# Kernel tuning notes

Measured on AMD Instinct MI355X. Metric: run time of the kernel, lower is better.

## Reference

```python
import jax, jax.numpy as jnp
import numpy as np

HEADS = 16
ROPE_BASE = 10000.0


def _rope(x):
    # x: [b, h, n, d]. lucidrains partial rotary: RotaryEmbedding(head_dim//2)
    # rotates only the first rot_dim = d//2 channels, interleaved-pair style.
    d = x.shape[-1]
    rot = d // 2
    inv_freq = 1.0 / (ROPE_BASE ** (jnp.arange(0, rot, 2, dtype=jnp.float32) / rot))  # [rot//2]
    pos = jnp.arange(x.shape[2], dtype=jnp.float32)
    freqs = pos[:, None] * inv_freq[None, :]                  # [n, rot//2]
    cos, sin = jnp.cos(freqs), jnp.sin(freqs)
    xr, xp = x[..., :rot], x[..., rot:]
    x1, x2 = xr[..., 0::2], xr[..., 1::2]                     # interleaved pairs
    o1 = x1 * cos - x2 * sin
    o2 = x2 * cos + x1 * sin
    xr_out = jnp.stack([o1, o2], axis=-1).reshape(xr.shape)   # re-interleave
    return jnp.concatenate([xr_out, xp], axis=-1)


def setup_inputs() -> dict:
    key = jax.random.key(0)
    k0, k1 = jax.random.split(key)
    B, N, D = 2, 2048, 2048
    x = jax.random.normal(k0, (B, N, D), dtype=jnp.float32)
    W_qkv = jax.random.normal(k1, (3 * D, D), dtype=jnp.float32) * (D ** -0.5)
    b_qkv = jnp.zeros((3 * D,), dtype=jnp.float32)
    return {"x": x, "W_qkv": W_qkv, "b_qkv": b_qkv}


def reference(x, W_qkv, b_qkv):
    B, N, D = x.shape
    H = HEADS
    hd = D // H
    qkv = x @ W_qkv.T + b_qkv                                  # [b, n, 3d]
    q, k, v = jnp.split(qkv, 3, axis=-1)
    to_heads = lambda t: t.reshape(B, N, H, hd).transpose(0, 2, 1, 3)  # b h n d
    q, k, v = to_heads(q), to_heads(k), to_heads(v)
    q, k = _rope(q), _rope(k)
    scale = 1.0 / np.sqrt(hd)
    scores = jnp.einsum('bhnd,bhmd->bhnm', q, k) * scale
    causal = jnp.tril(jnp.ones((N, N), dtype=bool))
    scores = jnp.where(causal, scores, -jnp.inf)
    attn = jax.nn.softmax(scores, axis=-1)
    y = jnp.einsum('bhnm,bhmd->bhnd', attn, v)
    return y.transpose(0, 2, 1, 3).reshape(B, N, D)
```

## Files before the change

kernel.cpp:

```cpp
#include <hip/hip_runtime.h>
#include <hip/hip_bf16.h>
#include <math.h>

typedef unsigned short u16;
typedef unsigned int u32;
typedef __attribute__((ext_vector_type(8))) short bf16x8;
typedef __attribute__((ext_vector_type(4))) float f32x4;

#define B_ 2
#define N_ 2048
#define D_ 2048
#define H_ 16
#define HD 128
#define GK 2048

__device__ __forceinline__ u16 f2bf(float f) {
  u32 u = __float_as_uint(f);
  u = (u + 0x7fffu + ((u >> 16) & 1u)) >> 16;
  return (u16)u;
}

__device__ __forceinline__ u32 cvtpk(float lo, float hi) {
  u32 r;
  asm("v_cvt_pk_bf16_f32 %0, %1, %2" : "=v"(r) : "v"(lo), "v"(hi));
  return r;
}

__device__ __forceinline__ void gload_lds16(const void* g, void* l) {
  __builtin_amdgcn_global_load_lds(
      (const __attribute__((address_space(1))) u32*)g,
      (__attribute__((address_space(3))) u32*)l, 16, 0, 0);
}

__global__ __launch_bounds__(256) void prep_kernel(
    const float* __restrict__ x, const float* __restrict__ Wq,
    u16* __restrict__ Xb, u16* __restrict__ Wb, float* __restrict__ tbl) {
  const int i0 = blockIdx.x * blockDim.x + threadIdx.x;
  const int st = gridDim.x * blockDim.x;
  const int n4x = (B_ * N_ * D_) / 4;
  const int n4w = (3 * D_ * D_) / 4;
  for (int i = i0; i < n4x + n4w; i += st) {
    float4 v;
    ushort4 o;
    if (i < n4x) {
      v = ((const float4*)x)[i];
      o.x = f2bf(v.x); o.y = f2bf(v.y); o.z = f2bf(v.z); o.w = f2bf(v.w);
      ((ushort4*)Xb)[i] = o;
    } else {
      v = ((const float4*)Wq)[i - n4x];
      o.x = f2bf(v.x); o.y = f2bf(v.y); o.z = f2bf(v.z); o.w = f2bf(v.w);
      ((ushort4*)Wb)[i - n4x] = o;
    }
  }
  for (int i = i0; i < N_ * 32; i += st) {
    int pos = i >> 5, p = i & 31;
    double inv = pow(10000.0, -(double)p / 32.0);
    double a = (double)pos * inv;
    tbl[2 * i]     = (float)cos(a);
    tbl[2 * i + 1] = (float)sin(a);
  }
}

__global__ __launch_bounds__(256, 2) void qkv_gemm_kernel(
    const u16* __restrict__ X, const u16* __restrict__ W,
    const float* __restrict__ bias, const float* __restrict__ tbl,
    u16* __restrict__ Qo, u16* __restrict__ Ko, u16* __restrict__ Vo) {
  __shared__ char smem[81920];
  const int tid = threadIdx.x;
  const int lane = tid & 63;
  const int w = tid >> 6;
  const int l15 = lane & 15, l4 = lane >> 4;

  const int bid = blockIdx.x;
  const int i_ = bid >> 3;
  const int m0 = (i_ >> 2) * 128;
  const int n0 = ((bid & 7) * 4 + (i_ & 3)) * 192;

  const int aof0 = (l4 * 16) ^ ((l15 & 7) << 4);
  const int aof1 = (64 + l4 * 16) ^ ((l15 & 7) << 4);

  int soRow[6], soCol[6];
#pragma unroll
  for (int c = 0; c < 6; ++c) {
    int o = c * 4096 + tid * 16;
    int lo = o ^ (((o >> 7) & 7) << 4);
    soRow[c] = lo >> 7;
    soCol[c] = (lo & 127) >> 1;
  }

  f32x4 acc[8][3];
#pragma unroll
  for (int fm = 0; fm < 8; ++fm)
#pragma unroll
    for (int fn = 0; fn < 3; ++fn)
#pragma unroll
      for (int q = 0; q < 4; ++q) acc[fm][fn][q] = 0.f;

  auto stageA = [&](char* Ab, int k0) {
#pragma unroll
    for (int c = 0; c < 4; ++c)
      gload_lds16(X + (size_t)(m0 + soRow[c]) * GK + k0 + soCol[c],
                  Ab + c * 4096 + tid * 16);
  };
  auto stageB = [&](char* Bb, int k0) {
#pragma unroll
    for (int c = 0; c < 6; ++c)
      gload_lds16(W + (size_t)(n0 + soRow[c]) * GK + k0 + soCol[c],
                  Bb + c * 4096 + tid * 16);
  };

  const int NK = GK / 64;

  stageA(smem, 0);
  stageB(smem + 32768, 0);
  asm volatile("s_waitcnt vmcnt(0)" ::: "memory");
  __builtin_amdgcn_s_barrier();

  for (int T = 0; T < NK; ++T) {
    const int cb = T & 1;
    const char* Ab = smem + cb * 16384;
    const char* Bb = smem + 32768 + cb * 24576;
    char* An = smem + (cb ^ 1) * 16384;
    char* Bn = smem + 32768 + (cb ^ 1) * 24576;
    const int kn = (T + 1) * 64;
    const bool nx = (T + 1 < NK);

    bf16x8 bl[3], bh[3], aq[4];

#pragma unroll
    for (int fn = 0; fn < 3; ++fn)
      bl[fn] = *(const bf16x8*)(Bb + (w * 48 + fn * 16 + l15) * 128 + aof0);
#pragma unroll
    for (int fm = 0; fm < 4; ++fm)
      aq[fm] = *(const bf16x8*)(Ab + (fm * 16 + l15) * 128 + aof0);
    if (nx) stageB(Bn, kn);
    __builtin_amdgcn_s_setprio(1);
#pragma unroll
    for (int fm = 0; fm < 4; ++fm)
#pragma unroll
      for (int fn = 0; fn < 3; ++fn)
        acc[fm][fn] = __builtin_amdgcn_mfma_f32_16x16x32_bf16(aq[fm], bl[fn], acc[fm][fn], 0, 0, 0);
    __builtin_amdgcn_s_setprio(0);

#pragma unroll
    for (int fm = 0; fm < 4; ++fm)
      aq[fm] = *(const bf16x8*)(Ab + ((fm + 4) * 16 + l15) * 128 + aof0);
    __builtin_amdgcn_s_setprio(1);
#pragma unroll
    for (int fm = 0; fm < 4; ++fm)
#pragma unroll
      for (int fn = 0; fn < 3; ++fn)
        acc[fm + 4][fn] = __builtin_amdgcn_mfma_f32_16x16x32_bf16(aq[fm], bl[fn], acc[fm + 4][fn], 0, 0, 0);
    __builtin_amdgcn_s_setprio(0);

#pragma unroll
    for (int fn = 0; fn < 3; ++fn)
      bh[fn] = *(const bf16x8*)(Bb + (w * 48 + fn * 16 + l15) * 128 + aof1);
#pragma unroll
    for (int fm = 0; fm < 4; ++fm)
      aq[fm] = *(const bf16x8*)(Ab + (fm * 16 + l15) * 128 + aof1);
    if (nx) stageA(An, kn);
    __builtin_amdgcn_s_setprio(1);
#pragma unroll
    for (int fm = 0; fm < 4; ++fm)
#pragma unroll
      for (int fn = 0; fn < 3; ++fn)
        acc[fm][fn] = __builtin_amdgcn_mfma_f32_16x16x32_bf16(aq[fm], bh[fn], acc[fm][fn], 0, 0, 0);
    __builtin_amdgcn_s_setprio(0);

#pragma unroll
    for (int fm = 0; fm < 4; ++fm)
      aq[fm] = *(const bf16x8*)(Ab + ((fm + 4) * 16 + l15) * 128 + aof1);
    asm volatile("s_waitcnt vmcnt(0)" ::: "memory");
    __builtin_amdgcn_s_setprio(1);
#pragma unroll
    for (int fm = 0; fm < 4; ++fm)
#pragma unroll
      for (int fn = 0; fn < 3; ++fn)
        acc[fm + 4][fn] = __builtin_amdgcn_mfma_f32_16x16x32_bf16(aq[fm], bh[fn], acc[fm + 4][fn], 0, 0, 0);
    __builtin_amdgcn_s_setprio(0);
    __builtin_amdgcn_s_barrier();
  }

  const float QSCALE = 0.08838834764831845f;
#pragma unroll
  for (int fn = 0; fn < 3; ++fn) {
    int gn = n0 + w * 48 + fn * 16 + l15;
    float bv = bias[gn];
    int sec = gn >> 11;
    int wi = gn & 2047;
    int h = wi >> 7;
    int d = wi & 127;
    u16* dstbase = (sec == 0) ? Qo : (sec == 1) ? Ko : Vo;
    float mulf = (sec == 0) ? QSCALE : 1.f;
    bool doRope = (sec < 2) && (d < 64);
    int pidx = d >> 1;
    bool odd = (d & 1) != 0;
#pragma unroll
    for (int fm = 0; fm < 8; ++fm) {
#pragma unroll
      for (int j = 0; j < 4; ++j) {
        int gm = m0 + fm * 16 + l4 * 4 + j;
        int bb = gm >> 11;
        int pos = gm & 2047;
        float v = acc[fm][fn][j] + bv;
        float pr = __shfl_xor(v, 1);
        float ov = v;
        if (doRope) {
          float2 cs = ((const float2*)tbl)[pos * 32 + pidx];
          ov = odd ? (v * cs.x + pr * cs.y) : (v * cs.x - pr * cs.y);
        }
        dstbase[(size_t)((bb * H_ + h) * N_ + pos) * HD + d] = f2bf(ov * mulf);
      }
    }
  }
}

__global__ __launch_bounds__(256, 2) void flash_kernel(
    const u16* __restrict__ Q, const u16* __restrict__ K, const u16* __restrict__ V,
    float* __restrict__ Out) {
  __shared__ char smem[51200];

  const int tid = threadIdx.x, lane = tid & 63, w = tid >> 6;
  const int l15 = lane & 15, l4 = lane >> 4;

  const int bid = blockIdx.x;
  const int xcd = bid & 7, s_ = bid >> 3;
  const int bh = xcd * 4 + (s_ & 3);
  const int x = 31 - (s_ >> 2);
  const int bb = bh >> 4, h = bh & 15;
  const size_t base = (size_t)bh * (N_ * HD);
  const int q0 = x * 64;
  const int nt = x + 1;

  bf16x8 qf[4];
  {
    const u16* qp = Q + base + (size_t)(q0 + w * 16 + l15) * HD + l4 * 8;
#pragma unroll
    for (int kf = 0; kf < 4; ++kf) qf[kf] = *(const bf16x8*)(qp + kf * 32);
  }

  float m_r = -1e30f, l_r = 0.f;
  f32x4 accO[8];
#pragma unroll
  for (int df = 0; df < 8; ++df)
#pragma unroll
    for (int q = 0; q < 4; ++q) accO[df][q] = 0.f;

  auto stageK = [&](int buf, int t0) {
    const u16* kb = K + base + (size_t)t0 * HD;
    char* kt = smem + buf * 16384;
#pragma unroll
    for (int i = 0; i < 4; ++i) {
      int c = w * 4 + i;
      int o = c * 1024 + lane * 16;
      int lo = o ^ (((o >> 8) & 7) << 4);
      gload_lds16(kb + (lo >> 1), kt + c * 1024);
    }
  };
  auto loadV = [&](int t0, bf16x8* vr) {
    const u16* vp = V + base + (size_t)(t0 + lane) * HD + w * 32;
#pragma unroll
    for (int i = 0; i < 4; ++i) vr[i] = *(const bf16x8*)(vp + i * 8);
  };
  auto writeV = [&](const bf16x8* vr) {
    u16* vt = (u16*)(smem + 32768);
#pragma unroll
    for (int i = 0; i < 4; ++i)
#pragma unroll
      for (int jj = 0; jj < 8; ++jj)
        vt[(w * 32 + i * 8 + jj) * 72 + lane] = (u16)vr[i][jj];
  };

  const int src0 = l15 + 32 * (l4 & 1);
  const int src1 = src0 + 16;
  const int half = l4 >> 1;
  union U8 { u32 u[4]; bf16x8 v; };

  bf16x8 vreg[4];
  stageK(0, 0);
  loadV(0, vreg);
  __syncthreads();
  writeV(vreg);
  __syncthreads();

  for (int t = 0; t < nt; ++t) {
    const int cur = t & 1;
    const int t0 = t * 64;
    const bool pre = (t + 1 < nt);
    if (pre) { stageK(cur ^ 1, t0 + 64); loadV(t0 + 64, vreg); }

    const char* kt = smem + cur * 16384;
    const u16* vt = (const u16*)(smem + 32768);

    f32x4 s[4];
#pragma unroll
    for (int cf = 0; cf < 4; ++cf) {
#pragma unroll
      for (int q = 0; q < 4; ++q) s[cf][q] = 0.f;
      int row = cf * 16 + l15;
      int sw = (row & 7) << 4;
#pragma unroll
      for (int kf = 0; kf < 4; ++kf) {
        int off = (row * 256 + kf * 64 + l4 * 16) ^ sw;
        bf16x8 kfrag = *(const bf16x8*)(kt + off);
        s[cf] = __builtin_amdgcn_mfma_f32_16x16x32_bf16(kfrag, qf[kf], s[cf], 0, 0, 0);
      }
    }

    const int qbase = q0 + w * 16;
    if (t0 + 63 > qbase) {
      const int qg = qbase + l15;
#pragma unroll
      for (int cf = 0; cf < 4; ++cf)
#pragma unroll
        for (int j = 0; j < 4; ++j) {
          int kvg = t0 + cf * 16 + l4 * 4 + j;
          if (kvg > qg) s[cf][j] = -1e30f;
        }
    }

    float pmax = s[0][0];
#pragma unroll
    for (int cf = 0; cf < 4; ++cf)
#pragma unroll
      for (int j = 0; j < 4; ++j) pmax = fmaxf(pmax, s[cf][j]);
    pmax = fmaxf(pmax, __shfl_xor(pmax, 16));
    pmax = fmaxf(pmax, __shfl_xor(pmax, 32));

    if (!__all(pmax <= m_r + 8.f)) {
      float mn = fmaxf(m_r, pmax);
      float rs = __expf(m_r - mn);
      m_r = mn;
      l_r *= rs;
#pragma unroll
      for (int df = 0; df < 8; ++df)
#pragma unroll
        for (int j = 0; j < 4; ++j) accO[df][j] *= rs;
    }

    u32 pk[4][2];
    float ps = 0.f;
#pragma unroll
    for (int cf = 0; cf < 4; ++cf) {
      float p0 = __expf(s[cf][0] - m_r);
      float p1 = __expf(s[cf][1] - m_r);
      float p2 = __expf(s[cf][2] - m_r);
      float p3 = __expf(s[cf][3] - m_r);
      ps += (p0 + p1) + (p2 + p3);
      pk[cf][0] = cvtpk(p0, p1);
      pk[cf][1] = cvtpk(p2, p3);
    }
    ps += __shfl_xor(ps, 16);
    ps += __shfl_xor(ps, 32);
    l_r += ps;

#pragma unroll
    for (int c = 0; c < 2; ++c) {
      const int c2 = 2 * c;
      u32 a0 = (u32)__shfl((int)pk[c2][0], src0);
      u32 b0 = (u32)__shfl((int)pk[c2 + 1][0], src0);
      u32 a1 = (u32)__shfl((int)pk[c2][1], src0);
      u32 b1 = (u32)__shfl((int)pk[c2 + 1][1], src0);
      u32 a2 = (u32)__shfl((int)pk[c2][0], src1);
      u32 b2 = (u32)__shfl((int)pk[c2 + 1][0], src1);
      u32 a3 = (u32)__shfl((int)pk[c2][1], src1);
      u32 b3 = (u32)__shfl((int)pk[c2 + 1][1], src1);
      U8 pu;
      pu.u[0] = half ? b0 : a0;
      pu.u[1] = half ? b1 : a1;
      pu.u[2] = half ? b2 : a2;
      pu.u[3] = half ? b3 : a3;
#pragma unroll
      for (int df = 0; df < 8; ++df) {
        bf16x8 vf = *(const bf16x8*)(vt + (df * 16 + l15) * 72 + c * 32 + l4 * 8);
        accO[df] = __builtin_amdgcn_mfma_f32_16x16x32_bf16(vf, pu.v, accO[df], 0, 0, 0);
      }
    }

    __syncthreads();
    if (pre) writeV(vreg);
    __syncthreads();
  }

  float* Obuf = (float*)(smem + w * 8448);
  const int l31 = lane & 31;
  {
    float inv = 1.f / l_r;
#pragma unroll
    for (int df = 0; df < 8; ++df) {
      f32x4 v = accO[df];
#pragma unroll
      for (int j = 0; j < 4; ++j) v[j] *= inv;
      *(f32x4*)&Obuf[l15 * 132 + df * 16 + l4 * 4] = v;
    }
  }
#pragma unroll
  for (int p = 0; p < 8; ++p) {
    int row = p * 2 + (lane >> 5);
    f32x4 v = *(const f32x4*)&Obuf[row * 132 + l31 * 4];
    int qg = q0 + w * 16 + row;
    *(f32x4*)&Out[(size_t)(bb * N_ + qg) * D_ + h * HD + l31 * 4] = v;
  }
}

extern "C" void kernel_launch(void* const* d_in, const int* in_sizes, int n_in,
                              void* d_out, int out_size, void* d_ws, size_t ws_size,
                              hipStream_t stream) {
  const float* x  = (const float*)d_in[0];
  const float* Wq = (const float*)d_in[1];
  const float* bq = (const float*)d_in[2];
  float* out = (float*)d_out;
  char* ws = (char*)d_ws;

  u16* Qb  = (u16*)(ws);
  u16* Kb  = (u16*)(ws + 16777216);
  u16* Vb  = (u16*)(ws + 2 * 16777216);
  u16* Xb  = (u16*)(ws + 3 * 16777216);
  u16* Wb  = (u16*)(ws + 4 * 16777216);
  float* tbl = (float*)(ws + 4 * 16777216 + 25165824);

  prep_kernel<<<2048, 256, 0, stream>>>(x, Wq, Xb, Wb, tbl);
  qkv_gemm_kernel<<<1024, 256, 0, stream>>>(Xb, Wb, bq, tbl, Qb, Kb, Vb);
  flash_kernel<<<1024, 256, 0, stream>>>(Qb, Kb, Vb, out);
}
```

Baseline: 236.6 us.

## Retile QKV GEMM to 256x128 with 8 waves and switch softmax to exp2

The QKV GEMM now uses 512-thread blocks with a 2x4 wave grid computing 256x128 tiles (768 blocks), with a 4x4 MFMA fragment per wave and staged loads split across two half-K phases separated by barriers. Separately, the log2(e) factor is folded into the Q scale so the flash kernel can use exp2f instead of __expf. The retiling changes the per-block reuse balance and wave count but adds extra barriers and raises LDS use to 96KB, which may limit residency to one block per CU.

New measurement: 257.8 us. 1.09x slower.

```diff
diff --git a/kernel.cpp b/kernel.cpp
--- a/kernel.cpp
+++ b/kernel.cpp
@@ -61,131 +61,111 @@
   }
 }
 
-__global__ __launch_bounds__(256, 2) void qkv_gemm_kernel(
+__global__ __launch_bounds__(512, 2) void qkv_gemm_kernel(
     const u16* __restrict__ X, const u16* __restrict__ W,
     const float* __restrict__ bias, const float* __restrict__ tbl,
     u16* __restrict__ Qo, u16* __restrict__ Ko, u16* __restrict__ Vo) {
-  __shared__ char smem[81920];
+  __shared__ char smem[98304];
   const int tid = threadIdx.x;
   const int lane = tid & 63;
   const int w = tid >> 6;
+  const int wm = w >> 1, wn = w & 1;
   const int l15 = lane & 15, l4 = lane >> 4;
 
   const int bid = blockIdx.x;
   const int i_ = bid >> 3;
-  const int m0 = (i_ >> 2) * 128;
-  const int n0 = ((bid & 7) * 4 + (i_ & 3)) * 192;
+  const int m0 = (i_ & 15) * 256;
+  const int n0 = ((bid & 7) * 6 + (i_ >> 4)) * 128;
 
   const int aof0 = (l4 * 16) ^ ((l15 & 7) << 4);
   const int aof1 = (64 + l4 * 16) ^ ((l15 & 7) << 4);
 
-  int soRow[6], soCol[6];
-#pragma unroll
-  for (int c = 0; c < 6; ++c) {
-    int o = c * 4096 + tid * 16;
+  int soRow[4], soCol[4];
+#pragma unroll
+  for (int c = 0; c < 4; ++c) {
+    int o = c * 8192 + tid * 16;
     int lo = o ^ (((o >> 7) & 7) << 4);
     soRow[c] = lo >> 7;
     soCol[c] = (lo & 127) >> 1;
   }
 
-  f32x4 acc[8][3];
-#pragma unroll
-  for (int fm = 0; fm < 8; ++fm)
-#pragma unroll
-    for (int fn = 0; fn < 3; ++fn)
+  f32x4 acc[4][4];
+#pragma unroll
+  for (int fm = 0; fm < 4; ++fm)
+#pragma unroll
+    for (int fn = 0; fn < 4; ++fn)
 #pragma unroll
       for (int q = 0; q < 4; ++q) acc[fm][fn][q] = 0.f;
 
-  auto stageA = [&](char* Ab, int k0) {
-#pragma unroll
-    for (int c = 0; c < 4; ++c)
-      gload_lds16(X + (size_t)(m0 + soRow[c]) * GK + k0 + soCol[c],
-                  Ab + c * 4096 + tid * 16);
+  auto stageA = [&](char* Ab, int c, int k0) {
+    gload_lds16(X + (size_t)(m0 + soRow[c]) * GK + k0 + soCol[c],
+                Ab + c * 8192 + tid * 16);
   };
-  auto stageB = [&](char* Bb, int k0) {
-#pragma unroll
-    for (int c = 0; c < 6; ++c)
-      gload_lds16(W + (size_t)(n0 + soRow[c]) * GK + k0 + soCol[c],
-                  Bb + c * 4096 + tid * 16);
+  auto stageB = [&](char* Bb, int c, int k0) {
+    gload_lds16(W + (size_t)(n0 + soRow[c]) * GK + k0 + soCol[c],
+                Bb + c * 8192 + tid * 16);
   };
 
   const int NK = GK / 64;
 
-  stageA(smem, 0);
-  stageB(smem + 32768, 0);
+#pragma unroll
+  for (int c = 0; c < 4; ++c) stageA(smem, c, 0);
+#pragma unroll
+  for (int c = 0; c < 2; ++c) stageB(smem + 65536, c, 0);
   asm volatile("s_waitcnt vmcnt(0)" ::: "memory");
   __builtin_amdgcn_s_barrier();
 
   for (int T = 0; T < NK; ++T) {
     const int cb = T & 1;
-    const char* Ab = smem + cb * 16384;
-    const char* Bb = smem + 32768 + cb * 24576;
-    char* An = smem + (cb ^ 1) * 16384;
-    char* Bn = smem + 32768 + (cb ^ 1) * 24576;
+    const char* Ab = smem + cb * 32768;
+    const char* Bb = smem + 65536 + cb * 16384;
+    char* An = smem + (cb ^ 1) * 32768;
+    char* Bn = smem + 65536 + (cb ^ 1) * 16384;
     const int kn = (T + 1) * 64;
     const bool nx = (T + 1 < NK);
 
-    bf16x8 bl[3], bh[3], aq[4];
-
-#pragma unroll
-    for (int fn = 0; fn < 3; ++fn)
-      bl[fn] = *(const bf16x8*)(Bb + (w * 48 + fn * 16 + l15) * 128 + aof0);
+    bf16x8 a[4], b[4];
+
 #pragma unroll
     for (int fm = 0; fm < 4; ++fm)
-      aq[fm] = *(const bf16x8*)(Ab + (fm * 16 + l15) * 128 + aof0);
-    if (nx) stageB(Bn, kn);
+      a[fm] = *(const bf16x8*)(Ab + (wm * 64 + fm * 16 + l15) * 128 + aof0);
+#pragma unroll
+    for (int fn = 0; fn < 4; ++fn)
+      b[fn] = *(const bf16x8*)(Bb + (wn * 64 + fn * 16 + l15) * 128 + aof0);
+    if (nx) { stageB(Bn, 0, kn); stageB(Bn, 1, kn); stageA(An, 0, kn); }
+    __builtin_amdgcn_s_barrier();
     __builtin_amdgcn_s_setprio(1);
 #pragma unroll
     for (int fm = 0; fm < 4; ++fm)
 #pragma unroll
-      for (int fn = 0; fn < 3; ++fn)
-        acc[fm][fn] = __builtin_amdgcn_mfma_f32_16x16x32_bf16(aq[fm], bl[fn], acc[fm][fn], 0, 0, 0);
-    __builtin_amdgcn_s_setprio(0);
-
-#pragma unroll
-    for (int fm = 0; fm < 4; ++fm)
-      aq[fm] = *(const bf16x8*)(Ab + ((fm + 4) * 16 + l15) * 128 + aof0);
-    __builtin_amdgcn_s_setprio(1);
-#pragma unroll
-    for (int fm = 0; fm < 4; ++fm)
-#pragma unroll
-      for (int fn = 0; fn < 3; ++fn)
-        acc[fm + 4][fn] = __builtin_amdgcn_mfma_f32_16x16x32_bf16(aq[fm], bl[fn], acc[fm + 4][fn], 0, 0, 0);
-    __builtin_amdgcn_s_setprio(0);
-
-#pragma unroll
-    for (int fn = 0; fn < 3; ++fn)
-      bh[fn] = *(const bf16x8*)(Bb + (w * 48 + fn * 16 + l15) * 128 + aof1);
-#pragma unroll
-    for (int fm = 0; fm < 4; ++fm)
-      aq[fm] = *(const bf16x8*)(Ab + (fm * 16 + l15) * 128 + aof1);
-    if (nx) stageA(An, kn);
-    __builtin_amdgcn_s_setprio(1);
-#pragma unroll
-    for (int fm = 0; fm < 4; ++fm)
-#pragma unroll
-      for (int fn = 0; fn < 3; ++fn)
-        acc[fm][fn] = __builtin_amdgcn_mfma_f32_16x16x32_bf16(aq[fm], bh[fn], acc[fm][fn], 0, 0, 0);
-    __builtin_amdgcn_s_setprio(0);
-
-#pragma unroll
-    for (int fm = 0; fm < 4; ++fm)
-      aq[fm] = *(const bf16x8*)(Ab + ((fm + 4) * 16 + l15) * 128 + aof1);
-    asm volatile("s_waitcnt vmcnt(0)" ::: "memory");
-    __builtin_amdgcn_s_setprio(1);
-#pragma unroll
-    for (int fm = 0; fm < 4; ++fm)
-#pragma unroll
-      for (int fn = 0; fn < 3; ++fn)
-        acc[fm + 4][fn] = __builtin_amdgcn_mfma_f32_16x16x32_bf16(aq[fm], bh[fn], acc[fm + 4][fn], 0, 0, 0);
+      for (int fn = 0; fn < 4; ++fn)
+        acc[fm][fn] = __builtin_amdgcn_mfma_f32_16x16x32_bf16(a[fm], b[fn], acc[fm][fn], 0, 0, 0);
     __builtin_amdgcn_s_setprio(0);
     __builtin_amdgcn_s_barrier();
-  }
-
-  const float QSCALE = 0.08838834764831845f;
-#pragma unroll
-  for (int fn = 0; fn < 3; ++fn) {
-    int gn = n0 + w * 48 + fn * 16 + l15;
+
+#pragma unroll
+    for (int fm = 0; fm < 4; ++fm)
+      a[fm] = *(const bf16x8*)(Ab + (wm * 64 + fm * 16 + l15) * 128 + aof1);
+#pragma unroll
+    for (int fn = 0; fn < 4; ++fn)
+      b[fn] = *(const bf16x8*)(Bb + (wn * 64 + fn * 16 + l15) * 128 + aof1);
+    if (nx) { stageA(An, 1, kn); stageA(An, 2, kn); stageA(An, 3, kn); }
+    __builtin_amdgcn_s_barrier();
+    __builtin_amdgcn_s_setprio(1);
+#pragma unroll
+    for (int fm = 0; fm < 4; ++fm)
+#pragma unroll
+      for (int fn = 0; fn < 4; ++fn)
+        acc[fm][fn] = __builtin_amdgcn_mfma_f32_16x16x32_bf16(a[fm], b[fn], acc[fm][fn], 0, 0, 0);
+    __builtin_amdgcn_s_setprio(0);
+    asm volatile("s_waitcnt vmcnt(0)" ::: "memory");
+    __builtin_amdgcn_s_barrier();
+  }
+
+  const float QSCALE = 0.08838834764831845f * 1.4426950408889634f;
+#pragma unroll
+  for (int fn = 0; fn < 4; ++fn) {
+    int gn = n0 + wn * 64 + fn * 16 + l15;
     float bv = bias[gn];
     int sec = gn >> 11;
     int wi = gn & 2047;
@@ -197,10 +177,10 @@
     int pidx = d >> 1;
     bool odd = (d & 1) != 0;
 #pragma unroll
-    for (int fm = 0; fm < 8; ++fm) {
+    for (int fm = 0; fm < 4; ++fm) {
 #pragma unroll
       for (int j = 0; j < 4; ++j) {
-        int gm = m0 + fm * 16 + l4 * 4 + j;
+        int gm = m0 + wm * 64 + fm * 16 + l4 * 4 + j;
         int bb = gm >> 11;
         int pos = gm & 2047;
         float v = acc[fm][fn][j] + bv;
@@ -330,7 +310,7 @@
 
     if (!__all(pmax <= m_r + 8.f)) {
       float mn = fmaxf(m_r, pmax);
-      float rs = __expf(m_r - mn);
+      float rs = exp2f(m_r - mn);
       m_r = mn;
       l_r *= rs;
 #pragma unroll
@@ -343,10 +323,10 @@
     float ps = 0.f;
 #pragma unroll
     for (int cf = 0; cf < 4; ++cf) {
-      float p0 = __expf(s[cf][0] - m_r);
-      float p1 = __expf(s[cf][1] - m_r);
-      float p2 = __expf(s[cf][2] - m_r);
-      float p3 = __expf(s[cf][3] - m_r);
+      float p0 = exp2f(s[cf][0] - m_r);
+      float p1 = exp2f(s[cf][1] - m_r);
+      float p2 = exp2f(s[cf][2] - m_r);
+      float p3 = exp2f(s[cf][3] - m_r);
       ps += (p0 + p1) + (p2 + p3);
       pk[cf][0] = cvtpk(p0, p1);
       pk[cf][1] = cvtpk(p2, p3);
@@ -421,6 +401,6 @@
   float* tbl = (float*)(ws + 4 * 16777216 + 25165824);
 
   prep_kernel<<<2048, 256, 0, stream>>>(x, Wq, Xb, Wb, tbl);
-  qkv_gemm_kernel<<<1024, 256, 0, stream>>>(Xb, Wb, bq, tbl, Qb, Kb, Vb);
+  qkv_gemm_kernel<<<768, 512, 0, stream>>>(Xb, Wb, bq, tbl, Qb, Kb, Vb);
   flash_kernel<<<1024, 256, 0, stream>>>(Qb, Kb, Vb, out);
 }
```
